# Kernel tuning notes

Hardware: AMD Instinct MI355X
Metric: run time of the kernel (lower is better)

Reference implementation:

```python
import jax, jax.numpy as jnp
import numpy as np

N_ROWS = 65536  # number of rows of the sparse input matrix


def setup_inputs() -> dict:
    key = jax.random.key(0)
    k1, k2, k3, k4, k5 = jax.random.split(key, 5)
    nnz, d_in, d_out = 524288, 512, 512
    rows = jax.random.randint(k1, (nnz,), 0, N_ROWS, dtype=jnp.int64)
    cols = jax.random.randint(k2, (nnz,), 0, d_in, dtype=jnp.int64)
    values = jax.random.normal(k3, (nnz,), dtype=jnp.float32)
    weight = jax.random.normal(k4, (d_out, d_in), dtype=jnp.float32) * (1.0 / np.sqrt(d_in))
    bound = 1.0 / np.sqrt(d_in)
    bias = jax.random.uniform(k5, (d_out,), minval=-bound, maxval=bound, dtype=jnp.float32)
    return {"rows": rows, "cols": cols, "values": values, "weight": weight, "bias": bias}


def reference(rows, cols, values, weight, bias):
    # y = sparse_input @ weight.T + bias
    # Each nonzero (r, c, v) contributes v * weight[:, c] to output row r.
    # weight: [d_out, d_in]; gather columns -> [nnz, d_out], segment-sum by row.
    contrib = values[:, None] * weight.T[cols]          # [nnz, d_out]
    y = jax.ops.segment_sum(contrib, rows, num_segments=N_ROWS)  # [N, d_out]
    return y + bias
```

## Files before the change

kernel.cpp:

```cpp
#include <hip/hip_runtime.h>
#include <hip/hip_bf16.h>

#define D 512
#define NROWS 65536
#define NBINS 256
#define RPB 256
#define P1B 1024
#define SEGCAP 16
#define MAXBLK1 512
#define RCAP 32
#define OVFCAP 4096

typedef float f32x4 __attribute__((ext_vector_type(4)));

__global__ __launch_bounds__(256) void k_phase1(const float* __restrict__ w,
                                                __hip_bfloat16* __restrict__ wt,
                                                const int* __restrict__ rows,
                                                const int* __restrict__ cols,
                                                const float* __restrict__ vals, int nnz, int nblk1,
                                                uint2* __restrict__ gBin, int* __restrict__ gBinCnt,
                                                int* __restrict__ ovf_cnt, uint4* __restrict__ ovf) {
    int b = blockIdx.x, t = threadIdx.x;
    if (b < 256) {
        __shared__ float tile[32][33];
        int bx = b & 15, by = b >> 4;
        int tx = t & 31, ty = t >> 5;
        for (int i = ty; i < 32; i += 8)
            tile[i][tx] = w[(by * 32 + i) * D + bx * 32 + tx];
        __syncthreads();
        for (int i = ty; i < 32; i += 8)
            wt[(bx * 32 + i) * D + by * 32 + tx] = __float2bfloat16(tile[tx][i]);
        return;
    }
    __shared__ int  binCnt[NBINS];
    __shared__ uint2 binBuf[NBINS][SEGCAP];
    b -= 256;
    binCnt[t] = 0;
    __syncthreads();
    int base = b * P1B;
    int end = base + P1B; if (end > nnz) end = nnz;
    for (int i = base + t; i < end; i += 256) {
        int r = rows[i], c = cols[i];
        unsigned vb = __float_as_uint(vals[i]);
        int bin = r >> 8;
        int pos = atomicAdd(&binCnt[bin], 1);
        if (pos < SEGCAP) {
            binBuf[bin][pos] = make_uint2(((unsigned)r << 9) | (unsigned)c, vb);
        } else {
            int o = atomicAdd(ovf_cnt, 1);
            if (o < OVFCAP) ovf[o] = make_uint4((unsigned)r, (unsigned)c, vb, 0u);
        }
    }
    __syncthreads();
    for (int idx = t; idx < NBINS * SEGCAP; idx += 256) {
        int bin = idx >> 4, slot = idx & (SEGCAP - 1);
        int cnt = binCnt[bin]; if (cnt > SEGCAP) cnt = SEGCAP;
        if (slot < cnt)
            gBin[((size_t)b * NBINS + bin) * SEGCAP + slot] = binBuf[bin][slot];
        if (slot == 0) gBinCnt[b * NBINS + bin] = cnt;
    }
}

#define ACC8(wb, vv)                                   \
    do {                                               \
        f32x4 w0, w1;                                  \
        w0.x = __uint_as_float((wb).x << 16);          \
        w0.y = __uint_as_float((wb).x & 0xffff0000u);  \
        w0.z = __uint_as_float((wb).y << 16);          \
        w0.w = __uint_as_float((wb).y & 0xffff0000u);  \
        w1.x = __uint_as_float((wb).z << 16);          \
        w1.y = __uint_as_float((wb).z & 0xffff0000u);  \
        w1.z = __uint_as_float((wb).w << 16);          \
        w1.w = __uint_as_float((wb).w & 0xffff0000u);  \
        a0 += (vv) * w0;                               \
        a1 += (vv) * w1;                               \
    } while (0)

__global__ __launch_bounds__(1024) void k_binspmm(const uint2* __restrict__ gBin,
                                                  const int* __restrict__ gBinCnt, int nblk1,
                                                  const uint4* __restrict__ wt4,
                                                  const f32x4* __restrict__ bias4,
                                                  f32x4* __restrict__ out,
                                                  int* __restrict__ ovf_cnt,
                                                  uint4* __restrict__ ovf) {
    __shared__ int  segCnt[MAXBLK1];
    __shared__ int  cursor[RPB];
    __shared__ uint2 rowBuf[RPB][RCAP];
    int bin = blockIdx.x, t = threadIdx.x;
    int wv = t >> 6, lane = t & 63;
    if (t < MAXBLK1) segCnt[t] = (t < nblk1) ? gBinCnt[t * NBINS + bin] : 0;
    if (t < RPB) cursor[t] = 0;
    __syncthreads();
    for (int idx = t; idx < nblk1 * SEGCAP; idx += 1024) {
        int blk = idx >> 4, slot = idx & (SEGCAP - 1);
        if (slot < segCnt[blk]) {
            uint2 p = gBin[((size_t)blk * NBINS + bin) * SEGCAP + slot];
            int r = (int)(p.x >> 9) & (RPB - 1);
            int pos = atomicAdd(&cursor[r], 1);
            if (pos < RCAP) {
                rowBuf[r][pos] = make_uint2(p.x & 511u, p.y);
            } else {
                int o = atomicAdd(ovf_cnt, 1);
                if (o < OVFCAP)
                    ovf[o] = make_uint4(p.x >> 9, p.x & 511u, p.y, 0u);
            }
        }
    }
    __syncthreads();
    f32x4 bb0 = bias4[lane * 2];
    f32x4 bb1 = bias4[lane * 2 + 1];
    int novf = *ovf_cnt;
    if (novf > OVFCAP) novf = OVFCAP;
    for (int rloc = wv; rloc < RPB; rloc += 16) {
        int cnt = cursor[rloc]; if (cnt > RCAP) cnt = RCAP;
        f32x4 a0 = bb0, a1 = bb1;
        for (int s = 0; s < cnt; s += 4) {
            int i1 = (s + 1 < cnt) ? s + 1 : s;
            int i2 = (s + 2 < cnt) ? s + 2 : s;
            int i3 = (s + 3 < cnt) ? s + 3 : s;
            uint2 p0 = rowBuf[rloc][s];
            uint2 p1 = rowBuf[rloc][i1];
            uint2 p2 = rowBuf[rloc][i2];
            uint2 p3 = rowBuf[rloc][i3];
            float v0 = __uint_as_float(p0.y);
            float v1 = (s + 1 < cnt) ? __uint_as_float(p1.y) : 0.f;
            float v2 = (s + 2 < cnt) ? __uint_as_float(p2.y) : 0.f;
            float v3 = (s + 3 < cnt) ? __uint_as_float(p3.y) : 0.f;
            uint4 wb0 = wt4[(size_t)p0.x * 64 + lane];
            uint4 wb1 = wt4[(size_t)p1.x * 64 + lane];
            uint4 wb2 = wt4[(size_t)p2.x * 64 + lane];
            uint4 wb3 = wt4[(size_t)p3.x * 64 + lane];
            ACC8(wb0, v0);
            ACC8(wb1, v1);
            ACC8(wb2, v2);
            ACC8(wb3, v3);
        }
        int row = (bin << 8) + rloc;
        if (novf > 0) {
            for (int e = 0; e < novf; ++e) {
                uint4 p = ovf[e];
                if ((int)p.x == row) {
                    float v = __uint_as_float(p.z);
                    uint4 wb = wt4[(size_t)p.y * 64 + lane];
                    ACC8(wb, v);
                }
            }
        }
        f32x4* op = out + (size_t)row * (D / 4);
        op[lane * 2]     = a0;
        op[lane * 2 + 1] = a1;
    }
}

__global__ void k_init_bias(const float* __restrict__ bias, float* __restrict__ out, int total) {
    int i = blockIdx.x * blockDim.x + threadIdx.x;
    if (i < total) out[i] = bias[i & (D - 1)];
}

__global__ void k_atomic_spmm(const int* __restrict__ rows, const int* __restrict__ cols,
                              const float* __restrict__ vals, int nnz,
                              const float* __restrict__ w, float* __restrict__ out) {
    int wid = (int)((blockIdx.x * blockDim.x + threadIdx.x) >> 6);
    if (wid >= nnz) return;
    int lane = threadIdx.x & 63;
    int r = rows[wid];
    int c = cols[wid];
    float v = vals[wid];
    float* op = out + (size_t)r * D + lane * 8;
#pragma unroll
    for (int k = 0; k < 8; ++k) {
        float wv = w[(size_t)(lane * 8 + k) * D + c];
        atomicAdd(&op[k], v * wv);
    }
}

extern "C" void kernel_launch(void* const* d_in, const int* in_sizes, int n_in,
                              void* d_out, int out_size, void* d_ws, size_t ws_size,
                              hipStream_t stream) {
    const int*   rows   = (const int*)d_in[0];
    const int*   cols   = (const int*)d_in[1];
    const float* vals   = (const float*)d_in[2];
    const float* weight = (const float*)d_in[3];
    const float* bias   = (const float*)d_in[4];
    float*       out    = (float*)d_out;
    const int nnz = in_sizes[0];
    const int nblk1 = (nnz + P1B - 1) / P1B;

    char* ws = (char*)d_ws;
    size_t off = 0;
    auto alloc = [&](size_t bytes) -> void* {
        off = (off + 255) & ~(size_t)255;
        void* p = ws + off;
        off += bytes;
        return p;
    };
    __hip_bfloat16* wT = (__hip_bfloat16*)alloc((size_t)D * D * sizeof(__hip_bfloat16));
    int*   ovf_cnt = (int*)  alloc(256);
    uint4* ovf     = (uint4*)alloc((size_t)OVFCAP * sizeof(uint4));
    uint2* gBin    = (uint2*)alloc((size_t)MAXBLK1 * NBINS * SEGCAP * sizeof(uint2));
    int*   gBinCnt = (int*)  alloc((size_t)MAXBLK1 * NBINS * sizeof(int));
    const size_t need_full = off;

    if (need_full <= ws_size && nblk1 <= MAXBLK1) {
        hipMemsetAsync(ovf_cnt, 0, sizeof(int), stream);
        k_phase1<<<256 + nblk1, 256, 0, stream>>>(weight, wT, rows, cols, vals, nnz, nblk1,
                                                  gBin, gBinCnt, ovf_cnt, ovf);
        k_binspmm<<<NBINS, 1024, 0, stream>>>(gBin, gBinCnt, nblk1, (const uint4*)wT,
                                              (const f32x4*)bias, (f32x4*)out, ovf_cnt, ovf);
    } else {
        k_init_bias<<<(out_size + 255) / 256, 256, 0, stream>>>(bias, out, out_size);
        k_atomic_spmm<<<((size_t)nnz * 64 + 255) / 256, 256, 0, stream>>>(rows, cols, vals, nnz, weight, out);
    }
}
```

Baseline: 59.61 us.

## Split binned SpMM into CSR bucketing kernel and per-row wave SpMM kernel

The fused bin-then-accumulate kernel is split in two. The first kernel sorts binned nonzeros into per-row buckets in LDS and writes those buckets plus per-row counts to global memory. The second kernel launches one wavefront per output row across many small blocks, and broadcasts each row's column/value pairs with readlane instead of LDS reads. The goal is better load balance and more parallelism than 256 large blocks that each loop over 256 rows. The cost is an extra launch and a global round trip of the full fixed-capacity bucket array.

```diff
diff --git a/kernel.cpp b/kernel.cpp
--- a/kernel.cpp
+++ b/kernel.cpp
@@ -61,6 +61,44 @@
     }
 }
 
+__global__ __launch_bounds__(1024) void k_csr(const uint2* __restrict__ gBin,
+                                              const int* __restrict__ gBinCnt, int nblk1,
+                                              uint2* __restrict__ bucket,
+                                              int* __restrict__ cnt,
+                                              int* __restrict__ ovf_cnt,
+                                              uint4* __restrict__ ovf) {
+    __shared__ int  segCnt[MAXBLK1];
+    __shared__ int  cursor[RPB];
+    __shared__ uint2 rowBuf[RPB][RCAP];
+    int bin = blockIdx.x, t = threadIdx.x;
+    if (t < MAXBLK1) segCnt[t] = (t < nblk1) ? gBinCnt[t * NBINS + bin] : 0;
+    if (t < RPB) cursor[t] = 0;
+    __syncthreads();
+    for (int idx = t; idx < nblk1 * SEGCAP; idx += 1024) {
+        int blk = idx >> 4, slot = idx & (SEGCAP - 1);
+        if (slot < segCnt[blk]) {
+            uint2 p = gBin[((size_t)blk * NBINS + bin) * SEGCAP + slot];
+            int r = (int)(p.x >> 9) & (RPB - 1);
+            int pos = atomicAdd(&cursor[r], 1);
+            if (pos < RCAP) {
+                rowBuf[r][pos] = make_uint2(p.x & 511u, p.y);
+            } else {
+                int o = atomicAdd(ovf_cnt, 1);
+                if (o < OVFCAP)
+                    ovf[o] = make_uint4(p.x >> 9, p.x & 511u, p.y, 0u);
+            }
+        }
+    }
+    __syncthreads();
+    uint2* bb = bucket + (size_t)bin * RPB * RCAP;
+    for (int k = t; k < RPB * RCAP; k += 1024)
+        bb[k] = ((const uint2*)rowBuf)[k];
+    if (t < RPB) {
+        int c = cursor[t]; if (c > RCAP) c = RCAP;
+        cnt[bin * RPB + t] = c;
+    }
+}
+
 #define ACC8(wb, vv)                                   \
     do {                                               \
         f32x4 w0, w1;                                  \
@@ -76,80 +114,57 @@
         a1 += (vv) * w1;                               \
     } while (0)
 
-__global__ __launch_bounds__(1024) void k_binspmm(const uint2* __restrict__ gBin,
-                                                  const int* __restrict__ gBinCnt, int nblk1,
-                                                  const uint4* __restrict__ wt4,
-                                                  const f32x4* __restrict__ bias4,
-                                                  f32x4* __restrict__ out,
-                                                  int* __restrict__ ovf_cnt,
-                                                  uint4* __restrict__ ovf) {
-    __shared__ int  segCnt[MAXBLK1];
-    __shared__ int  cursor[RPB];
-    __shared__ uint2 rowBuf[RPB][RCAP];
-    int bin = blockIdx.x, t = threadIdx.x;
-    int wv = t >> 6, lane = t & 63;
-    if (t < MAXBLK1) segCnt[t] = (t < nblk1) ? gBinCnt[t * NBINS + bin] : 0;
-    if (t < RPB) cursor[t] = 0;
-    __syncthreads();
-    for (int idx = t; idx < nblk1 * SEGCAP; idx += 1024) {
-        int blk = idx >> 4, slot = idx & (SEGCAP - 1);
-        if (slot < segCnt[blk]) {
-            uint2 p = gBin[((size_t)blk * NBINS + bin) * SEGCAP + slot];
-            int r = (int)(p.x >> 9) & (RPB - 1);
-            int pos = atomicAdd(&cursor[r], 1);
-            if (pos < RCAP) {
-                rowBuf[r][pos] = make_uint2(p.x & 511u, p.y);
-            } else {
-                int o = atomicAdd(ovf_cnt, 1);
-                if (o < OVFCAP)
-                    ovf[o] = make_uint4(p.x >> 9, p.x & 511u, p.y, 0u);
+__global__ __launch_bounds__(256) void k_spmm(const int* __restrict__ cnts,
+                                              const uint2* __restrict__ bucket,
+                                              const uint4* __restrict__ wt4,
+                                              const f32x4* __restrict__ bias4,
+                                              f32x4* __restrict__ out,
+                                              const int* __restrict__ ovf_cnt,
+                                              const uint4* __restrict__ ovf) {
+    int wid = (int)((blockIdx.x * blockDim.x + threadIdx.x) >> 6);
+    int row = __builtin_amdgcn_readfirstlane(wid);
+    int lane = threadIdx.x & 63;
+    f32x4 a0 = bias4[lane * 2];
+    f32x4 a1 = bias4[lane * 2 + 1];
+    int cnt = cnts[row];
+    int novf = *ovf_cnt;
+    if (cnt > RCAP) cnt = RCAP;
+    uint2 mypair = make_uint2(0u, 0u);
+    if (lane < cnt) mypair = bucket[(size_t)row * RCAP + lane];
+    int nb4 = (cnt + 3) >> 2;
+    for (int b4 = 0; b4 < nb4; ++b4) {
+        int s = b4 << 2;
+        unsigned c0 = (unsigned)__builtin_amdgcn_readlane((int)mypair.x, s);
+        unsigned c1 = (unsigned)__builtin_amdgcn_readlane((int)mypair.x, s + 1);
+        unsigned c2 = (unsigned)__builtin_amdgcn_readlane((int)mypair.x, s + 2);
+        unsigned c3 = (unsigned)__builtin_amdgcn_readlane((int)mypair.x, s + 3);
+        float v0 = __uint_as_float((unsigned)__builtin_amdgcn_readlane((int)mypair.y, s));
+        float v1 = __uint_as_float((unsigned)__builtin_amdgcn_readlane((int)mypair.y, s + 1));
+        float v2 = __uint_as_float((unsigned)__builtin_amdgcn_readlane((int)mypair.y, s + 2));
+        float v3 = __uint_as_float((unsigned)__builtin_amdgcn_readlane((int)mypair.y, s + 3));
+        uint4 wb0 = wt4[(size_t)c0 * 64 + lane];
+        uint4 wb1 = wt4[(size_t)c1 * 64 + lane];
+        uint4 wb2 = wt4[(size_t)c2 * 64 + lane];
+        uint4 wb3 = wt4[(size_t)c3 * 64 + lane];
+        ACC8(wb0, v0);
+        ACC8(wb1, v1);
+        ACC8(wb2, v2);
+        ACC8(wb3, v3);
+    }
+    if (novf > 0) {
+        if (novf > OVFCAP) novf = OVFCAP;
+        for (int e = 0; e < novf; ++e) {
+            uint4 p = ovf[e];
+            if ((int)p.x == row) {
+                float v = __uint_as_float(p.z);
+                uint4 wb = wt4[(size_t)p.y * 64 + lane];
+                ACC8(wb, v);
             }
         }
     }
-    __syncthreads();
-    f32x4 bb0 = bias4[lane * 2];
-    f32x4 bb1 = bias4[lane * 2 + 1];
-    int novf = *ovf_cnt;
-    if (novf > OVFCAP) novf = OVFCAP;
-    for (int rloc = wv; rloc < RPB; rloc += 16) {
-        int cnt = cursor[rloc]; if (cnt > RCAP) cnt = RCAP;
-        f32x4 a0 = bb0, a1 = bb1;
-        for (int s = 0; s < cnt; s += 4) {
-            int i1 = (s + 1 < cnt) ? s + 1 : s;
-            int i2 = (s + 2 < cnt) ? s + 2 : s;
-            int i3 = (s + 3 < cnt) ? s + 3 : s;
-            uint2 p0 = rowBuf[rloc][s];
-            uint2 p1 = rowBuf[rloc][i1];
-            uint2 p2 = rowBuf[rloc][i2];
-            uint2 p3 = rowBuf[rloc][i3];
-            float v0 = __uint_as_float(p0.y);
-            float v1 = (s + 1 < cnt) ? __uint_as_float(p1.y) : 0.f;
-            float v2 = (s + 2 < cnt) ? __uint_as_float(p2.y) : 0.f;
-            float v3 = (s + 3 < cnt) ? __uint_as_float(p3.y) : 0.f;
-            uint4 wb0 = wt4[(size_t)p0.x * 64 + lane];
-            uint4 wb1 = wt4[(size_t)p1.x * 64 + lane];
-            uint4 wb2 = wt4[(size_t)p2.x * 64 + lane];
-            uint4 wb3 = wt4[(size_t)p3.x * 64 + lane];
-            ACC8(wb0, v0);
-            ACC8(wb1, v1);
-            ACC8(wb2, v2);
-            ACC8(wb3, v3);
-        }
-        int row = (bin << 8) + rloc;
-        if (novf > 0) {
-            for (int e = 0; e < novf; ++e) {
-                uint4 p = ovf[e];
-                if ((int)p.x == row) {
-                    float v = __uint_as_float(p.z);
-                    uint4 wb = wt4[(size_t)p.y * 64 + lane];
-                    ACC8(wb, v);
-                }
-            }
-        }
-        f32x4* op = out + (size_t)row * (D / 4);
-        op[lane * 2]     = a0;
-        op[lane * 2 + 1] = a1;
-    }
+    f32x4* op = out + (size_t)row * (D / 4);
+    op[lane * 2]     = a0;
+    op[lane * 2 + 1] = a1;
 }
 
 __global__ void k_init_bias(const float* __restrict__ bias, float* __restrict__ out, int total) {
@@ -199,13 +214,16 @@
     uint4* ovf     = (uint4*)alloc((size_t)OVFCAP * sizeof(uint4));
     uint2* gBin    = (uint2*)alloc((size_t)MAXBLK1 * NBINS * SEGCAP * sizeof(uint2));
     int*   gBinCnt = (int*)  alloc((size_t)MAXBLK1 * NBINS * sizeof(int));
+    uint2* bucket  = (uint2*)alloc((size_t)NROWS * RCAP * sizeof(uint2));
+    int*   cnt     = (int*)  alloc((size_t)NROWS * sizeof(int));
     const size_t need_full = off;
 
     if (need_full <= ws_size && nblk1 <= MAXBLK1) {
         hipMemsetAsync(ovf_cnt, 0, sizeof(int), stream);
         k_phase1<<<256 + nblk1, 256, 0, stream>>>(weight, wT, rows, cols, vals, nnz, nblk1,
                                                   gBin, gBinCnt, ovf_cnt, ovf);
-        k_binspmm<<<NBINS, 1024, 0, stream>>>(gBin, gBinCnt, nblk1, (const uint4*)wT,
+        k_csr<<<NBINS, 1024, 0, stream>>>(gBin, gBinCnt, nblk1, bucket, cnt, ovf_cnt, ovf);
+        k_spmm<<<NROWS / 4, 256, 0, stream>>>(cnt, bucket, (const uint4*)wT,
                                               (const f32x4*)bias, (f32x4*)out, ovf_cnt, ovf);
     } else {
         k_init_bias<<<(out_size + 255) / 256, 256, 0, stream>>>(bias, out, out_size);
```

Measured after the change: 64.97 us. 9.0% more time.
